# Kernel tuning notes

Measured on AMD Instinct MI355X. Metric: run time of the kernel, lower is better.

Reference implementation:

```python
import jax, jax.numpy as jnp
import numpy as np

B, O, L, E = 8, 4, 1024, 1024
BETA = 512
NSEG = 12
OUT = 1


def setup_inputs() -> dict:
    key = jax.random.key(0)
    ks = jax.random.split(key, 8)
    hidden = jax.random.normal(ks[0], (B, O, L, E), jnp.float32)
    # strictly increasing boundaries in (1, L), shared across the O options (as in the torch code)
    raw = jnp.sort(jax.random.randint(ks[1], (B, NSEG), 2, L - NSEG), axis=-1)
    idx = raw + jnp.arange(NSEG, dtype=raw.dtype)
    s = 0.02
    Wp = jax.random.normal(ks[2], (E, 2 * BETA), jnp.float32) * s
    bp = jnp.zeros((2 * BETA,), jnp.float32)
    Wa0 = jax.random.normal(ks[3], (2 * BETA, BETA), jnp.float32) * s
    ba0 = jnp.zeros((BETA,), jnp.float32)
    Wa = jax.random.normal(ks[4], (BETA, BETA), jnp.float32) * s
    ba = jnp.zeros((BETA,), jnp.float32)
    Wl0 = jax.random.normal(ks[5], (8 * BETA, BETA), jnp.float32) * s
    bl0 = jnp.zeros((BETA,), jnp.float32)
    Wl = jax.random.normal(ks[6], (BETA, OUT), jnp.float32) * s
    bl = jnp.zeros((OUT,), jnp.float32)
    return dict(hidden=hidden, idx=idx, Wp=Wp, bp=bp, Wa0=Wa0, ba0=ba0,
                Wa=Wa, ba=ba, Wl0=Wl0, bl0=bl0, Wl=Wl, bl=bl)


def _seg_mean(P, starts, ends):
    # P: [B,O,L+1,E] exclusive prefix sums; starts/ends: [B,K] token offsets.
    s = jnp.take_along_axis(P, starts[:, None, :, None], axis=2)
    e = jnp.take_along_axis(P, ends[:, None, :, None], axis=2)
    cnt = (ends - starts).astype(P.dtype)[:, None, :, None]
    return (e - s) / cnt  # [B,O,K,E]


def _get_param(x, Wp, bp):
    e = 1.0 + jax.nn.relu(x @ Wp + bp)
    a, b = jnp.split(e, 2, axis=-1)
    return a, b


def _attn_pool(a, b, Wa0, ba0, Wa, ba):
    # attention-weighted reduction over axis -2 (the 'logic' operator)
    h = jax.nn.relu(jnp.concatenate([a, b], axis=-1) @ Wa0 + ba0)
    w = jax.nn.softmax(h @ Wa + ba, axis=-2)
    return (w * a).sum(axis=-2), (w * b).sum(axis=-2)


def reference(hidden, idx, Wp, bp, Wa0, ba0, Wa, ba, Wl0, bl0, Wl, bl):
    # ---- init_embed: ragged segment means via prefix sums (one pass, no host syncs)
    P = jnp.concatenate([jnp.zeros_like(hidden[:, :, :1]),
                         jnp.cumsum(hidden, axis=2)], axis=2)  # [B,O,L+1,E]
    ones = jnp.ones((idx.shape[0], 1), idx.dtype)
    starts_c = jnp.concatenate([ones, idx[:, :NSEG - 3]], axis=1)  # [B, NSEG-2]
    ends_c = idx[:, :NSEG - 2]
    ctx = _seg_mean(P, starts_c, ends_c)                                # [B,O,Nc,E]
    q = _seg_mean(P, idx[:, NSEG - 3:NSEG - 2], idx[:, NSEG - 2:NSEG - 1])[:, :, 0]
    o = _seg_mean(P, idx[:, NSEG - 2:NSEG - 1], idx[:, NSEG - 1:NSEG])[:, :, 0]
    allc = _seg_mean(P, ones, idx[:, NSEG - 3:NSEG - 2])[:, :, 0]       # [B,O,E]
    # ---- beta params for context segments
    a_c, b_c = _get_param(ctx, Wp, bp)                                  # [B,O,Nc,BETA]
    # intersection over segments
    ia, ib = _attn_pool(a_c, b_c, Wa0, ba0, Wa, ba)                     # [B,O,BETA]
    # renew: pair each segment with the intersection, pool over the pair axis
    pa = jnp.stack([a_c, jnp.broadcast_to(ia[:, :, None, :], a_c.shape)], axis=-2)
    pb = jnp.stack([b_c, jnp.broadcast_to(ib[:, :, None, :], b_c.shape)], axis=-2)
    na, nb = _attn_pool(pa, pb, Wa0, ba0, Wa, ba)                       # [B,O,Nc,BETA]
    # union: invert, attention-pool over segments, invert back
    ua, ub = _attn_pool(1.0 / na, 1.0 / nb, Wa0, ba0, Wa, ba)
    ua, ub = 1.0 / ua, 1.0 / ub                                         # [B,O,BETA]
    # ---- beta params for question / option / whole-context spans
    a_q, b_q = _get_param(q, Wp, bp)
    a_o, b_o = _get_param(o, Wp, bp)
    a_ac, b_ac = _get_param(allc, Wp, bp)
    # ---- classify head: concat 4 beta embeddings -> 8*BETA -> MLP -> logits
    cat = jnp.concatenate([ua, ub, a_ac, b_ac, a_o, b_o, a_q, b_q], axis=-1)
    h = jax.nn.relu(cat @ Wl0 + bl0)
    return h @ Wl + bl  # [B,O,OUT]
```

## Files before the change

kernel.cpp:

```cpp
#include <hip/hip_runtime.h>
#include <hip/hip_bf16.h>

#define B_    8
#define O_    4
#define L_    1024
#define E_    1024
#define BETA_ 512
#define NSEG_ 12
#define BO_   32

enum : size_t {
  WS_S       = 0,
  WS_P1      = WS_S   + (size_t)BO_ * 12 * E_,
  WS_H1      = WS_P1  + (size_t)BO_ * 13 * E_,
  WS_T1      = WS_H1  + (size_t)BO_ * 10 * BETA_,
  WS_H2      = WS_T1  + (size_t)BO_ * 10 * BETA_,
  WS_T2      = WS_H2  + (size_t)BO_ * BETA_,
  WS_H3      = WS_T2  + (size_t)BO_ * BETA_,
  WS_T3      = WS_H3  + (size_t)BO_ * 10 * BETA_,
  WS_HF      = WS_T3  + (size_t)BO_ * 10 * BETA_,
  WS_ACC_END = WS_HF  + (size_t)BO_ * BETA_,
  WS_X       = WS_ACC_END,
  WS_IAB     = WS_X   + (size_t)BO_ * 13 * E_,
  WS_RN      = WS_IAB + (size_t)BO_ * 2 * BETA_,
  WS_CAT     = WS_RN  + (size_t)BO_ * 10 * E_,
  WS_END     = WS_CAT + (size_t)BO_ * 8 * BETA_,
};

__device__ __forceinline__ float relu_(float v) { return v > 0.f ? v : 0.f; }

__global__ void k1_segsum(const float* __restrict__ hidden, const int* __restrict__ idx,
                          float* __restrict__ S) {
    const int bo = blockIdx.y;
    const int b = bo >> 2;
    int cuts[13];
    cuts[0] = 1;
#pragma unroll
    for (int i = 0; i < 12; ++i) cuts[i + 1] = idx[b * NSEG_ + i];
    const int rows = L_ / 64;
    const int l0 = blockIdx.x * rows;
    const int l1 = l0 + rows;
    int lo = l0 < 1 ? 1 : l0;
    const int hi = l1 < cuts[12] ? l1 : cuts[12];
    if (lo >= hi) return;
    const int e4 = threadIdx.x << 2;
    const float* base = hidden + (size_t)bo * (L_ * E_) + e4;
    int j = 0;
    while (j < 11 && cuts[j + 1] <= lo) ++j;
    int l = lo;
    while (l < hi) {
        const int e2 = (j < 11 && cuts[j + 1] < hi) ? cuts[j + 1] : hi;
        float sx = 0.f, sy = 0.f, sz = 0.f, sw = 0.f;
        for (; l < e2; ++l) {
            const float4 v = *reinterpret_cast<const float4*>(base + (size_t)l * E_);
            sx += v.x; sy += v.y; sz += v.z; sw += v.w;
        }
        float* sp = S + ((size_t)bo * 12 + j) * E_ + e4;
        atomicAdd(sp + 0, sx);
        atomicAdd(sp + 1, sy);
        atomicAdd(sp + 2, sz);
        atomicAdd(sp + 3, sw);
        ++j;
    }
}

__global__ void k2_means(const float* __restrict__ S, const int* __restrict__ idx,
                         float* __restrict__ X) {
    const int bo = blockIdx.x;
    const int b = bo >> 2;
    int cuts[13];
    cuts[0] = 1;
#pragma unroll
    for (int i = 0; i < 12; ++i) cuts[i + 1] = idx[b * NSEG_ + i];
    const int e4 = threadIdx.x << 2;
    const float4* Sp = reinterpret_cast<const float4*>(S + (size_t)bo * 12 * E_ + e4);
    float4* Xp = reinterpret_cast<float4*>(X + (size_t)bo * 13 * E_ + e4);
    float ax = 0.f, ay = 0.f, az = 0.f, aw = 0.f;
#pragma unroll
    for (int r = 0; r < 12; ++r) {
        const float4 s = Sp[r * (E_ / 4)];
        const float inv = 1.0f / (float)(cuts[r + 1] - cuts[r]);
        float4 m;
        m.x = s.x * inv; m.y = s.y * inv; m.z = s.z * inv; m.w = s.w * inv;
        Xp[r * (E_ / 4)] = m;
        if (r < 10) { ax += s.x; ay += s.y; az += s.z; aw += s.w; }
    }
    const float inva = 1.0f / (float)(cuts[10] - 1);
    float4 m;
    m.x = ax * inva; m.y = ay * inva; m.z = az * inva; m.w = aw * inva;
    Xp[12 * (E_ / 4)] = m;
}

template<int M, int K, int N, int KC, int BOG, int XF, int XBO>
__global__ __launch_bounds__(256) void gemm_sk(
    const float* __restrict__ Xb, const float* __restrict__ xbias,
    const float* __restrict__ W, float* __restrict__ OUT) {
    const int k0  = blockIdx.x * KC;
    const int bo0 = blockIdx.y * BOG;
    const int c   = blockIdx.z * 256 + threadIdx.x;
    __shared__ __align__(16) float xs[BOG * M * KC];
    for (int i = threadIdx.x; i < BOG * M * KC; i += 256) {
        const int kk = i % KC;
        const int rm = i / KC;
        const int m  = rm % M;
        const int b  = rm / M;
        float v = Xb[(size_t)(bo0 + b) * XBO + (size_t)m * K + k0 + kk];
        if constexpr (XF >= 1) {
            v += xbias[k0 + kk];
            v = relu_(v);
            if constexpr (XF == 1) v += 1.f;
        }
        xs[i] = v;
    }
    __syncthreads();
    float acc[BOG][M];
#pragma unroll
    for (int b = 0; b < BOG; ++b)
#pragma unroll
        for (int m = 0; m < M; ++m) acc[b][m] = 0.f;
    const float* __restrict__ wp = W + (size_t)k0 * N + c;
    for (int k4 = 0; k4 < KC / 4; ++k4) {
        const float w0 = wp[(size_t)(4 * k4 + 0) * N];
        const float w1 = wp[(size_t)(4 * k4 + 1) * N];
        const float w2 = wp[(size_t)(4 * k4 + 2) * N];
        const float w3 = wp[(size_t)(4 * k4 + 3) * N];
#pragma unroll
        for (int b = 0; b < BOG; ++b) {
#pragma unroll
            for (int m = 0; m < M; ++m) {
                const float4 xv = *reinterpret_cast<const float4*>(&xs[(b * M + m) * KC + 4 * k4]);
                float a = acc[b][m];
                a = fmaf(xv.x, w0, a);
                a = fmaf(xv.y, w1, a);
                a = fmaf(xv.z, w2, a);
                a = fmaf(xv.w, w3, a);
                acc[b][m] = a;
            }
        }
    }
#pragma unroll
    for (int b = 0; b < BOG; ++b) {
        float* op = OUT + (size_t)(bo0 + b) * M * N + c;
#pragma unroll
        for (int m = 0; m < M; ++m) atomicAdd(op + (size_t)m * N, acc[b][m]);
    }
}

__global__ void __launch_bounds__(512) ep3_iab(
    const float* __restrict__ P1, const float* __restrict__ bp,
    const float* __restrict__ T1, const float* __restrict__ ba,
    float* __restrict__ IAB) {
    const int bo = blockIdx.x;
    const int c = threadIdx.x;
    const float bac = ba[c];
    float t[10];
#pragma unroll
    for (int j = 0; j < 10; ++j) t[j] = T1[((size_t)bo * 10 + j) * BETA_ + c] + bac;
    float m = t[0];
#pragma unroll
    for (int j = 1; j < 10; ++j) m = fmaxf(m, t[j]);
    float p[10], sw = 0.f;
#pragma unroll
    for (int j = 0; j < 10; ++j) { p[j] = expf(t[j] - m); sw += p[j]; }
    const float inv = 1.0f / sw;
    const float bpa = bp[c], bpb = bp[BETA_ + c];
    const float* Pp = P1 + (size_t)bo * 13 * E_;
    float ia = 0.f, ib = 0.f;
#pragma unroll
    for (int j = 0; j < 10; ++j) {
        const float pj = p[j] * inv;
        const float ea = 1.f + relu_(Pp[(size_t)j * E_ + c] + bpa);
        const float eb = 1.f + relu_(Pp[(size_t)j * E_ + BETA_ + c] + bpb);
        ia = fmaf(pj, ea, ia);
        ib = fmaf(pj, eb, ib);
    }
    IAB[(size_t)bo * 1024 + c] = ia;
    IAB[(size_t)bo * 1024 + BETA_ + c] = ib;
}

__global__ void __launch_bounds__(512) ep5_rn(
    const float* __restrict__ P1, const float* __restrict__ bp,
    const float* __restrict__ T1, const float* __restrict__ T2,
    const float* __restrict__ ba, const float* __restrict__ IAB,
    float* __restrict__ RN) {
    const int bo = blockIdx.x;
    const int c = threadIdx.x;
    const float bac = ba[c];
    const float tI = T2[(size_t)bo * BETA_ + c] + bac;
    const float ia = IAB[(size_t)bo * 1024 + c];
    const float ib = IAB[(size_t)bo * 1024 + BETA_ + c];
    const float bpa = bp[c], bpb = bp[BETA_ + c];
    const float* Pp = P1 + (size_t)bo * 13 * E_;
#pragma unroll
    for (int j = 0; j < 10; ++j) {
        const float tj = T1[((size_t)bo * 10 + j) * BETA_ + c] + bac;
        const float m = fmaxf(tj, tI);
        const float e0 = expf(tj - m);
        const float e1 = expf(tI - m);
        const float inv = 1.0f / (e0 + e1);
        const float ea = 1.f + relu_(Pp[(size_t)j * E_ + c] + bpa);
        const float eb = 1.f + relu_(Pp[(size_t)j * E_ + BETA_ + c] + bpb);
        const float na = (e0 * ea + e1 * ia) * inv;
        const float nb = (e0 * eb + e1 * ib) * inv;
        RN[((size_t)bo * 10 + j) * E_ + c] = 1.0f / na;
        RN[((size_t)bo * 10 + j) * E_ + BETA_ + c] = 1.0f / nb;
    }
}

__global__ void __launch_bounds__(512) ep7_cat(
    const float* __restrict__ P1, const float* __restrict__ bp,
    const float* __restrict__ T3, const float* __restrict__ ba,
    const float* __restrict__ RN, float* __restrict__ CAT) {
    const int bo = blockIdx.x;
    const int c = threadIdx.x;
    const float bac = ba[c];
    float t[10];
#pragma unroll
    for (int j = 0; j < 10; ++j) t[j] = T3[((size_t)bo * 10 + j) * BETA_ + c] + bac;
    float m = t[0];
#pragma unroll
    for (int j = 1; j < 10; ++j) m = fmaxf(m, t[j]);
    float p[10], sw = 0.f;
#pragma unroll
    for (int j = 0; j < 10; ++j) { p[j] = expf(t[j] - m); sw += p[j]; }
    const float inv = 1.0f / sw;
    float uap = 0.f, ubp = 0.f;
#pragma unroll
    for (int j = 0; j < 10; ++j) {
        const float pj = p[j] * inv;
        uap = fmaf(pj, RN[((size_t)bo * 10 + j) * E_ + c], uap);
        ubp = fmaf(pj, RN[((size_t)bo * 10 + j) * E_ + BETA_ + c], ubp);
    }
    const float bpa = bp[c], bpb = bp[BETA_ + c];
    const float* Pp = P1 + (size_t)bo * 13 * E_;
    float* catp = CAT + (size_t)bo * 4096;
    catp[c] = 1.0f / uap;
    catp[BETA_ + c] = 1.0f / ubp;
    catp[1024 + c]          = 1.f + relu_(Pp[12 * E_ + c] + bpa);
    catp[1024 + BETA_ + c]  = 1.f + relu_(Pp[12 * E_ + BETA_ + c] + bpb);
    catp[2048 + c]          = 1.f + relu_(Pp[11 * E_ + c] + bpa);
    catp[2048 + BETA_ + c]  = 1.f + relu_(Pp[11 * E_ + BETA_ + c] + bpb);
    catp[3072 + c]          = 1.f + relu_(Pp[10 * E_ + c] + bpa);
    catp[3072 + BETA_ + c]  = 1.f + relu_(Pp[10 * E_ + BETA_ + c] + bpb);
}

__global__ void __launch_bounds__(512) k_final(
    const float* __restrict__ HF, const float* __restrict__ bl0,
    const float* __restrict__ Wl, const float* __restrict__ bl,
    float* __restrict__ out) {
    const int bo = blockIdx.x;
    const int c = threadIdx.x;
    float v = relu_(HF[(size_t)bo * BETA_ + c] + bl0[c]);
    float partial = v * Wl[c];
#pragma unroll
    for (int off = 32; off > 0; off >>= 1) partial += __shfl_down(partial, off, 64);
    __shared__ float red[8];
    if ((c & 63) == 0) red[c >> 6] = partial;
    __syncthreads();
    if (c == 0) {
        float s = 0.f;
#pragma unroll
        for (int i = 0; i < 8; ++i) s += red[i];
        out[bo] = s + bl[0];
    }
}

extern "C" void kernel_launch(void* const* d_in, const int* in_sizes, int n_in,
                              void* d_out, int out_size, void* d_ws, size_t ws_size,
                              hipStream_t stream) {
    const float* hidden = (const float*)d_in[0];
    const int* idx = (const int*)d_in[1];
    const float* Wp  = (const float*)d_in[2];
    const float* bp  = (const float*)d_in[3];
    const float* Wa0 = (const float*)d_in[4];
    const float* ba0 = (const float*)d_in[5];
    const float* Wa  = (const float*)d_in[6];
    const float* ba  = (const float*)d_in[7];
    const float* Wl0 = (const float*)d_in[8];
    const float* bl0 = (const float*)d_in[9];
    const float* Wl  = (const float*)d_in[10];
    const float* bl  = (const float*)d_in[11];
    float* ws = (float*)d_ws;
    float* S   = ws + WS_S;
    float* P1  = ws + WS_P1;
    float* H1  = ws + WS_H1;
    float* T1  = ws + WS_T1;
    float* H2  = ws + WS_H2;
    float* T2  = ws + WS_T2;
    float* H3  = ws + WS_H3;
    float* T3  = ws + WS_T3;
    float* HF  = ws + WS_HF;
    float* X   = ws + WS_X;
    float* IAB = ws + WS_IAB;
    float* RN  = ws + WS_RN;
    float* CAT = ws + WS_CAT;

    hipMemsetAsync(S, 0, (size_t)(WS_ACC_END - WS_S) * sizeof(float), stream);
    k1_segsum<<<dim3(64, BO_), 256, 0, stream>>>(hidden, idx, S);
    k2_means<<<BO_, 256, 0, stream>>>(S, idx, X);
    gemm_sk<13, 1024, 1024, 128, 2, 0, 13 * 1024>
        <<<dim3(8, 16, 4), 256, 0, stream>>>(X, nullptr, Wp, P1);
    gemm_sk<10, 1024, 512, 64, 2, 1, 13 * 1024>
        <<<dim3(16, 16, 2), 256, 0, stream>>>(P1, bp, Wa0, H1);
    gemm_sk<10, 512, 512, 64, 2, 2, 10 * 512>
        <<<dim3(8, 16, 2), 256, 0, stream>>>(H1, ba0, Wa, T1);
    ep3_iab<<<BO_, 512, 0, stream>>>(P1, bp, T1, ba, IAB);
    gemm_sk<1, 1024, 512, 128, 8, 0, 1024>
        <<<dim3(8, 4, 2), 256, 0, stream>>>(IAB, nullptr, Wa0, H2);
    gemm_sk<1, 512, 512, 64, 8, 2, 512>
        <<<dim3(8, 4, 2), 256, 0, stream>>>(H2, ba0, Wa, T2);
    ep5_rn<<<BO_, 512, 0, stream>>>(P1, bp, T1, T2, ba, IAB, RN);
    gemm_sk<10, 1024, 512, 64, 2, 0, 10 * 1024>
        <<<dim3(16, 16, 2), 256, 0, stream>>>(RN, nullptr, Wa0, H3);
    gemm_sk<10, 512, 512, 64, 2, 2, 10 * 512>
        <<<dim3(8, 16, 2), 256, 0, stream>>>(H3, ba0, Wa, T3);
    ep7_cat<<<BO_, 512, 0, stream>>>(P1, bp, T3, ba, RN, CAT);
    gemm_sk<1, 4096, 512, 64, 8, 0, 4096>
        <<<dim3(64, 4, 2), 256, 0, stream>>>(CAT, nullptr, Wl0, HF);
    k_final<<<BO_, 512, 0, stream>>>(HF, bl0, Wl, bl, (float*)d_out);
}
```

Baseline: 193.1 us.

## Fuse segment-mean and softmax epilogues into GEMM operand loads

Removes the k2_means, ep3_iab, ep5_rn and ep7_cat kernels. Their work now happens inside the shared-memory staging loop of gemm_sk, selected by new XF modes. The goal is to cut four kernel launches and the global-memory round trips for the X and CAT intermediates. IAB and RN are still written out as side outputs because later stages read them. In exchange, the softmax and segment-sum work is recomputed redundantly across grid blocks, the last GEMM's K-chunk size changes, and k_final now folds two elements per thread.

```diff
diff --git a/kernel.cpp b/kernel.cpp
--- a/kernel.cpp
+++ b/kernel.cpp
@@ -10,21 +10,19 @@
 #define BO_   32
 
 enum : size_t {
-  WS_S       = 0,
-  WS_P1      = WS_S   + (size_t)BO_ * 12 * E_,
-  WS_H1      = WS_P1  + (size_t)BO_ * 13 * E_,
-  WS_T1      = WS_H1  + (size_t)BO_ * 10 * BETA_,
-  WS_H2      = WS_T1  + (size_t)BO_ * 10 * BETA_,
-  WS_T2      = WS_H2  + (size_t)BO_ * BETA_,
-  WS_H3      = WS_T2  + (size_t)BO_ * BETA_,
-  WS_T3      = WS_H3  + (size_t)BO_ * 10 * BETA_,
-  WS_HF      = WS_T3  + (size_t)BO_ * 10 * BETA_,
-  WS_ACC_END = WS_HF  + (size_t)BO_ * BETA_,
-  WS_X       = WS_ACC_END,
-  WS_IAB     = WS_X   + (size_t)BO_ * 13 * E_,
-  WS_RN      = WS_IAB + (size_t)BO_ * 2 * BETA_,
-  WS_CAT     = WS_RN  + (size_t)BO_ * 10 * E_,
-  WS_END     = WS_CAT + (size_t)BO_ * 8 * BETA_,
+  WS_S    = 0,
+  WS_P1   = WS_S   + (size_t)BO_ * 12 * E_,
+  WS_H1   = WS_P1  + (size_t)BO_ * 13 * E_,
+  WS_T1   = WS_H1  + (size_t)BO_ * 10 * BETA_,
+  WS_H2   = WS_T1  + (size_t)BO_ * 10 * BETA_,
+  WS_T2   = WS_H2  + (size_t)BO_ * BETA_,
+  WS_H3   = WS_T2  + (size_t)BO_ * BETA_,
+  WS_T3   = WS_H3  + (size_t)BO_ * 10 * BETA_,
+  WS_HF   = WS_T3  + (size_t)BO_ * 10 * BETA_,
+  WS_ZEND = WS_HF  + (size_t)BO_ * BETA_,
+  WS_IAB  = WS_ZEND,
+  WS_RN   = WS_IAB + (size_t)BO_ * 2 * BETA_,
+  WS_END  = WS_RN  + (size_t)BO_ * 10 * E_,
 };
 
 __device__ __forceinline__ float relu_(float v) { return v > 0.f ? v : 0.f; }
@@ -64,55 +62,118 @@
     }
 }
 
-__global__ void k2_means(const float* __restrict__ S, const int* __restrict__ idx,
-                         float* __restrict__ X) {
-    const int bo = blockIdx.x;
-    const int b = bo >> 2;
-    int cuts[13];
-    cuts[0] = 1;
-#pragma unroll
-    for (int i = 0; i < 12; ++i) cuts[i + 1] = idx[b * NSEG_ + i];
-    const int e4 = threadIdx.x << 2;
-    const float4* Sp = reinterpret_cast<const float4*>(S + (size_t)bo * 12 * E_ + e4);
-    float4* Xp = reinterpret_cast<float4*>(X + (size_t)bo * 13 * E_ + e4);
-    float ax = 0.f, ay = 0.f, az = 0.f, aw = 0.f;
-#pragma unroll
-    for (int r = 0; r < 12; ++r) {
-        const float4 s = Sp[r * (E_ / 4)];
-        const float inv = 1.0f / (float)(cuts[r + 1] - cuts[r]);
-        float4 m;
-        m.x = s.x * inv; m.y = s.y * inv; m.z = s.z * inv; m.w = s.w * inv;
-        Xp[r * (E_ / 4)] = m;
-        if (r < 10) { ax += s.x; ay += s.y; az += s.z; aw += s.w; }
-    }
-    const float inva = 1.0f / (float)(cuts[10] - 1);
-    float4 m;
-    m.x = ax * inva; m.y = ay * inva; m.z = az * inva; m.w = aw * inva;
-    Xp[12 * (E_ / 4)] = m;
-}
-
 template<int M, int K, int N, int KC, int BOG, int XF, int XBO>
 __global__ __launch_bounds__(256) void gemm_sk(
     const float* __restrict__ Xb, const float* __restrict__ xbias,
-    const float* __restrict__ W, float* __restrict__ OUT) {
+    const float* __restrict__ W, float* __restrict__ OUT,
+    const float* __restrict__ A0, const float* __restrict__ A1,
+    const float* __restrict__ A2, const float* __restrict__ A3,
+    const float* __restrict__ A4, const float* __restrict__ A5,
+    float* __restrict__ SIDE, const int* __restrict__ idxp) {
     const int k0  = blockIdx.x * KC;
     const int bo0 = blockIdx.y * BOG;
     const int c   = blockIdx.z * 256 + threadIdx.x;
+    const int tid = threadIdx.x;
     __shared__ __align__(16) float xs[BOG * M * KC];
-    for (int i = threadIdx.x; i < BOG * M * KC; i += 256) {
+
+    float invc[12], invall;
+    if constexpr (XF == 3) {
+        int cuts[13];
+        cuts[0] = 1;
+        const int b0 = bo0 >> 2;
+#pragma unroll
+        for (int i = 0; i < 12; ++i) cuts[i + 1] = idxp[b0 * NSEG_ + i];
+#pragma unroll
+        for (int m = 0; m < 12; ++m) invc[m] = 1.0f / (float)(cuts[m + 1] - cuts[m]);
+        invall = 1.0f / (float)(cuts[10] - 1);
+    }
+
+    for (int i = tid; i < BOG * M * KC; i += 256) {
         const int kk = i % KC;
         const int rm = i / KC;
         const int m  = rm % M;
-        const int b  = rm / M;
-        float v = Xb[(size_t)(bo0 + b) * XBO + (size_t)m * K + k0 + kk];
-        if constexpr (XF >= 1) {
-            v += xbias[k0 + kk];
+        const int bb = rm / M;
+        const int bo = bo0 + bb;
+        const int k  = k0 + kk;
+        float v;
+        if constexpr (XF == 0) {
+            v = Xb[(size_t)bo * XBO + (size_t)m * K + k];
+        } else if constexpr (XF == 1 || XF == 2) {
+            v = Xb[(size_t)bo * XBO + (size_t)m * K + k] + xbias[k];
             v = relu_(v);
             if constexpr (XF == 1) v += 1.f;
+        } else if constexpr (XF == 3) {
+            if (m < 12) {
+                v = Xb[((size_t)bo * 12 + m) * E_ + k] * invc[m];
+            } else {
+                float s = 0.f;
+#pragma unroll
+                for (int r = 0; r < 10; ++r) s += Xb[((size_t)bo * 12 + r) * E_ + k];
+                v = s * invall;
+            }
+        } else if constexpr (XF == 4) {
+            const int col = k & 511, half = k >> 9;
+            const float bac = A2[col];
+            float t[10], mx = -1e30f;
+#pragma unroll
+            for (int j = 0; j < 10; ++j) {
+                t[j] = A0[((size_t)bo * 10 + j) * BETA_ + col] + bac;
+                mx = fmaxf(mx, t[j]);
+            }
+            float p[10], sw = 0.f;
+#pragma unroll
+            for (int j = 0; j < 10; ++j) { p[j] = expf(t[j] - mx); sw += p[j]; }
+            const float bpc = A3[half * BETA_ + col];
+            float acc = 0.f;
+#pragma unroll
+            for (int j = 0; j < 10; ++j) {
+                const float e = 1.f + relu_(A1[(size_t)bo * 13 * E_ + (size_t)j * E_ + half * BETA_ + col] + bpc);
+                acc = fmaf(p[j], e, acc);
+            }
+            v = acc / sw;
+            SIDE[(size_t)bo * 1024 + k] = v;
+        } else if constexpr (XF == 5) {
+            const int col = k & 511, half = k >> 9;
+            const int j = m;
+            const float bac = A4[col];
+            const float tj = A0[((size_t)bo * 10 + j) * BETA_ + col] + bac;
+            const float tI = A1[(size_t)bo * BETA_ + col] + bac;
+            const float mx = fmaxf(tj, tI);
+            const float e0 = expf(tj - mx);
+            const float e1 = expf(tI - mx);
+            const float iv = A2[(size_t)bo * 1024 + half * BETA_ + col];
+            const float ea = 1.f + relu_(A3[(size_t)bo * 13 * E_ + (size_t)j * E_ + half * BETA_ + col] + A5[half * BETA_ + col]);
+            v = (e0 + e1) / (e0 * ea + e1 * iv);
+            SIDE[((size_t)bo * 10 + j) * 1024 + k] = v;
+        } else {
+            if (k < 1024) {
+                const int col = k & 511, half = k >> 9;
+                const float bac = A3[col];
+                float t[10], mx = -1e30f;
+#pragma unroll
+                for (int j = 0; j < 10; ++j) {
+                    t[j] = A0[((size_t)bo * 10 + j) * BETA_ + col] + bac;
+                    mx = fmaxf(mx, t[j]);
+                }
+                float sw = 0.f, acc = 0.f;
+#pragma unroll
+                for (int j = 0; j < 10; ++j) {
+                    const float p = expf(t[j] - mx);
+                    sw += p;
+                    acc = fmaf(p, A1[((size_t)bo * 10 + j) * 1024 + half * BETA_ + col], acc);
+                }
+                v = sw / acc;
+            } else {
+                const int region = k >> 10;
+                const int row = (region == 1) ? 12 : (region == 2) ? 11 : 10;
+                const int col = k & 1023;
+                v = 1.f + relu_(A2[(size_t)bo * 13 * E_ + (size_t)row * E_ + col] + A4[col]);
+            }
         }
         xs[i] = v;
     }
     __syncthreads();
+
     float acc[BOG][M];
 #pragma unroll
     for (int b = 0; b < BOG; ++b)
@@ -146,123 +207,21 @@
     }
 }
 
-__global__ void __launch_bounds__(512) ep3_iab(
-    const float* __restrict__ P1, const float* __restrict__ bp,
-    const float* __restrict__ T1, const float* __restrict__ ba,
-    float* __restrict__ IAB) {
-    const int bo = blockIdx.x;
-    const int c = threadIdx.x;
-    const float bac = ba[c];
-    float t[10];
-#pragma unroll
-    for (int j = 0; j < 10; ++j) t[j] = T1[((size_t)bo * 10 + j) * BETA_ + c] + bac;
-    float m = t[0];
-#pragma unroll
-    for (int j = 1; j < 10; ++j) m = fmaxf(m, t[j]);
-    float p[10], sw = 0.f;
-#pragma unroll
-    for (int j = 0; j < 10; ++j) { p[j] = expf(t[j] - m); sw += p[j]; }
-    const float inv = 1.0f / sw;
-    const float bpa = bp[c], bpb = bp[BETA_ + c];
-    const float* Pp = P1 + (size_t)bo * 13 * E_;
-    float ia = 0.f, ib = 0.f;
-#pragma unroll
-    for (int j = 0; j < 10; ++j) {
-        const float pj = p[j] * inv;
-        const float ea = 1.f + relu_(Pp[(size_t)j * E_ + c] + bpa);
-        const float eb = 1.f + relu_(Pp[(size_t)j * E_ + BETA_ + c] + bpb);
-        ia = fmaf(pj, ea, ia);
-        ib = fmaf(pj, eb, ib);
-    }
-    IAB[(size_t)bo * 1024 + c] = ia;
-    IAB[(size_t)bo * 1024 + BETA_ + c] = ib;
-}
-
-__global__ void __launch_bounds__(512) ep5_rn(
-    const float* __restrict__ P1, const float* __restrict__ bp,
-    const float* __restrict__ T1, const float* __restrict__ T2,
-    const float* __restrict__ ba, const float* __restrict__ IAB,
-    float* __restrict__ RN) {
-    const int bo = blockIdx.x;
-    const int c = threadIdx.x;
-    const float bac = ba[c];
-    const float tI = T2[(size_t)bo * BETA_ + c] + bac;
-    const float ia = IAB[(size_t)bo * 1024 + c];
-    const float ib = IAB[(size_t)bo * 1024 + BETA_ + c];
-    const float bpa = bp[c], bpb = bp[BETA_ + c];
-    const float* Pp = P1 + (size_t)bo * 13 * E_;
-#pragma unroll
-    for (int j = 0; j < 10; ++j) {
-        const float tj = T1[((size_t)bo * 10 + j) * BETA_ + c] + bac;
-        const float m = fmaxf(tj, tI);
-        const float e0 = expf(tj - m);
-        const float e1 = expf(tI - m);
-        const float inv = 1.0f / (e0 + e1);
-        const float ea = 1.f + relu_(Pp[(size_t)j * E_ + c] + bpa);
-        const float eb = 1.f + relu_(Pp[(size_t)j * E_ + BETA_ + c] + bpb);
-        const float na = (e0 * ea + e1 * ia) * inv;
-        const float nb = (e0 * eb + e1 * ib) * inv;
-        RN[((size_t)bo * 10 + j) * E_ + c] = 1.0f / na;
-        RN[((size_t)bo * 10 + j) * E_ + BETA_ + c] = 1.0f / nb;
-    }
-}
-
-__global__ void __launch_bounds__(512) ep7_cat(
-    const float* __restrict__ P1, const float* __restrict__ bp,
-    const float* __restrict__ T3, const float* __restrict__ ba,
-    const float* __restrict__ RN, float* __restrict__ CAT) {
-    const int bo = blockIdx.x;
-    const int c = threadIdx.x;
-    const float bac = ba[c];
-    float t[10];
-#pragma unroll
-    for (int j = 0; j < 10; ++j) t[j] = T3[((size_t)bo * 10 + j) * BETA_ + c] + bac;
-    float m = t[0];
-#pragma unroll
-    for (int j = 1; j < 10; ++j) m = fmaxf(m, t[j]);
-    float p[10], sw = 0.f;
-#pragma unroll
-    for (int j = 0; j < 10; ++j) { p[j] = expf(t[j] - m); sw += p[j]; }
-    const float inv = 1.0f / sw;
-    float uap = 0.f, ubp = 0.f;
-#pragma unroll
-    for (int j = 0; j < 10; ++j) {
-        const float pj = p[j] * inv;
-        uap = fmaf(pj, RN[((size_t)bo * 10 + j) * E_ + c], uap);
-        ubp = fmaf(pj, RN[((size_t)bo * 10 + j) * E_ + BETA_ + c], ubp);
-    }
-    const float bpa = bp[c], bpb = bp[BETA_ + c];
-    const float* Pp = P1 + (size_t)bo * 13 * E_;
-    float* catp = CAT + (size_t)bo * 4096;
-    catp[c] = 1.0f / uap;
-    catp[BETA_ + c] = 1.0f / ubp;
-    catp[1024 + c]          = 1.f + relu_(Pp[12 * E_ + c] + bpa);
-    catp[1024 + BETA_ + c]  = 1.f + relu_(Pp[12 * E_ + BETA_ + c] + bpb);
-    catp[2048 + c]          = 1.f + relu_(Pp[11 * E_ + c] + bpa);
-    catp[2048 + BETA_ + c]  = 1.f + relu_(Pp[11 * E_ + BETA_ + c] + bpb);
-    catp[3072 + c]          = 1.f + relu_(Pp[10 * E_ + c] + bpa);
-    catp[3072 + BETA_ + c]  = 1.f + relu_(Pp[10 * E_ + BETA_ + c] + bpb);
-}
-
 __global__ void __launch_bounds__(512) k_final(
     const float* __restrict__ HF, const float* __restrict__ bl0,
     const float* __restrict__ Wl, const float* __restrict__ bl,
     float* __restrict__ out) {
     const int bo = blockIdx.x;
     const int c = threadIdx.x;
-    float v = relu_(HF[(size_t)bo * BETA_ + c] + bl0[c]);
-    float partial = v * Wl[c];
+    const float v1 = relu_(HF[(size_t)bo * BETA_ + c] + bl0[c]) * Wl[c];
+    const float v2 = relu_(HF[(size_t)bo * BETA_ + 256 + c] + bl0[256 + c]) * Wl[256 + c];
+    float partial = v1 + v2;
 #pragma unroll
     for (int off = 32; off > 0; off >>= 1) partial += __shfl_down(partial, off, 64);
     __shared__ float red[8];
     if ((c & 63) == 0) red[c >> 6] = partial;
     __syncthreads();
-    if (c == 0) {
-        float s = 0.f;
-#pragma unroll
-        for (int i = 0; i < 8; ++i) s += red[i];
-        out[bo] = s + bl[0];
-    }
+    if (c == 0) out[bo] = red[0] + red[1] + red[2] + red[3] + bl[0];
 }
 
 extern "C" void kernel_launch(void* const* d_in, const int* in_sizes, int n_in,
@@ -290,32 +249,27 @@
     float* H3  = ws + WS_H3;
     float* T3  = ws + WS_T3;
     float* HF  = ws + WS_HF;
-    float* X   = ws + WS_X;
     float* IAB = ws + WS_IAB;
     float* RN  = ws + WS_RN;
-    float* CAT = ws + WS_CAT;
-
-    hipMemsetAsync(S, 0, (size_t)(WS_ACC_END - WS_S) * sizeof(float), stream);
+    const float* NUL = nullptr;
+
+    hipMemsetAsync(S, 0, (size_t)WS_ZEND * sizeof(float), stream);
     k1_segsum<<<dim3(64, BO_), 256, 0, stream>>>(hidden, idx, S);
-    k2_means<<<BO_, 256, 0, stream>>>(S, idx, X);
-    gemm_sk<13, 1024, 1024, 128, 2, 0, 13 * 1024>
-        <<<dim3(8, 16, 4), 256, 0, stream>>>(X, nullptr, Wp, P1);
+    gemm_sk<13, 1024, 1024, 128, 2, 3, 0>
+        <<<dim3(8, 16, 4), 256, 0, stream>>>(S, NUL, Wp, P1, NUL, NUL, NUL, NUL, NUL, NUL, nullptr, idx);
     gemm_sk<10, 1024, 512, 64, 2, 1, 13 * 1024>
-        <<<dim3(16, 16, 2), 256, 0, stream>>>(P1, bp, Wa0, H1);
+        <<<dim3(16, 16, 2), 256, 0, stream>>>(P1, bp, Wa0, H1, NUL, NUL, NUL, NUL, NUL, NUL, nullptr, nullptr);
     gemm_sk<10, 512, 512, 64, 2, 2, 10 * 512>
-        <<<dim3(8, 16, 2), 256, 0, stream>>>(H1, ba0, Wa, T1);
-    ep3_iab<<<BO_, 512, 0, stream>>>(P1, bp, T1, ba, IAB);
-    gemm_sk<1, 1024, 512, 128, 8, 0, 1024>
-        <<<dim3(8, 4, 2), 256, 0, stream>>>(IAB, nullptr, Wa0, H2);
+        <<<dim3(8, 16, 2), 256, 0, stream>>>(H1, ba0, Wa, T1, NUL, NUL, NUL, NUL, NUL, NUL, nullptr, nullptr);
+    gemm_sk<1, 1024, 512, 128, 8, 4, 0>
+        <<<dim3(8, 4, 2), 256, 0, stream>>>(NUL, NUL, Wa0, H2, T1, P1, ba, bp, NUL, NUL, IAB, nullptr);
     gemm_sk<1, 512, 512, 64, 8, 2, 512>
-        <<<dim3(8, 4, 2), 256, 0, stream>>>(H2, ba0, Wa, T2);
-    ep5_rn<<<BO_, 512, 0, stream>>>(P1, bp, T1, T2, ba, IAB, RN);
-    gemm_sk<10, 1024, 512, 64, 2, 0, 10 * 1024>
-        <<<dim3(16, 16, 2), 256, 0, stream>>>(RN, nullptr, Wa0, H3);
+        <<<dim3(8, 4, 2), 256, 0, stream>>>(H2, ba0, Wa, T2, NUL, NUL, NUL, NUL, NUL, NUL, nullptr, nullptr);
+    gemm_sk<10, 1024, 512, 64, 2, 5, 0>
+        <<<dim3(16, 16, 2), 256, 0, stream>>>(NUL, NUL, Wa0, H3, T1, T2, IAB, P1, ba, bp, RN, nullptr);
     gemm_sk<10, 512, 512, 64, 2, 2, 10 * 512>
-        <<<dim3(8, 16, 2), 256, 0, stream>>>(H3, ba0, Wa, T3);
-    ep7_cat<<<BO_, 512, 0, stream>>>(P1, bp, T3, ba, RN, CAT);
-    gemm_sk<1, 4096, 512, 64, 8, 0, 4096>
-        <<<dim3(64, 4, 2), 256, 0, stream>>>(CAT, nullptr, Wl0, HF);
+        <<<dim3(8, 16, 2), 256, 0, stream>>>(H3, ba0, Wa, T3, NUL, NUL, NUL, NUL, NUL, NUL, nullptr, nullptr);
+    gemm_sk<1, 4096, 512, 128, 8, 6, 0>
+        <<<dim3(32, 4, 2), 256, 0, stream>>>(NUL, NUL, Wl0, HF, T3, RN, P1, ba, bp, NUL, nullptr, nullptr);
     k_final<<<BO_, 512, 0, stream>>>(HF, bl0, Wl, bl, (float*)d_out);
 }
```

New measurement: 189.4 us. Within noise of the previous version (-1.9%).
